# Performance work log

Measured on AMD Instinct MI355X. Metric: run time of the kernel, lower is better.

The kernel has to match this reference:

```python
import jax, jax.numpy as jnp
import numpy as np

N_GRAPHS = 8192
NODES_PER_GRAPH = 62
IN_CH = 4
HID = 64
NUM_CLASSES = 3
DEG = 8
N = N_GRAPHS * NODES_PER_GRAPH        # 507904 total nodes
E = N * DEG                            # 4063232 edges
BN_EPS = 1e-5


def setup_inputs() -> dict:
    key = jax.random.key(0)
    ks = jax.random.split(key, 24)

    def lin_w(k, i, o):
        return (jax.random.normal(k, (i, o), jnp.float32) / np.float32(np.sqrt(i)))

    inp = {
        "x": jax.random.normal(ks[0], (N, IN_CH), jnp.float32),
        "edge_src": jax.random.randint(ks[1], (E,), 0, N, dtype=jnp.int32),
        "edge_dst": jax.random.randint(ks[2], (E,), 0, N, dtype=jnp.int32),
        "num_graphs": N_GRAPHS,
        # conv1 MLP: Linear(4,64) -> ReLU -> Linear(64,64)
        "W1a": lin_w(ks[3], IN_CH, HID), "b1a": jnp.zeros((HID,), jnp.float32),
        "W1b": lin_w(ks[4], HID, HID),   "b1b": jnp.zeros((HID,), jnp.float32),
        "g1": jnp.ones((HID,), jnp.float32), "be1": jnp.zeros((HID,), jnp.float32),
        # conv2 MLP
        "W2a": lin_w(ks[5], HID, HID), "b2a": jnp.zeros((HID,), jnp.float32),
        "W2b": lin_w(ks[6], HID, HID), "b2b": jnp.zeros((HID,), jnp.float32),
        "g2": jnp.ones((HID,), jnp.float32), "be2": jnp.zeros((HID,), jnp.float32),
        # conv3 MLP
        "W3a": lin_w(ks[7], HID, HID), "b3a": jnp.zeros((HID,), jnp.float32),
        "W3b": lin_w(ks[8], HID, HID), "b3b": jnp.zeros((HID,), jnp.float32),
        "g3": jnp.ones((HID,), jnp.float32), "be3": jnp.zeros((HID,), jnp.float32),
        # final classifier fc2 (fc1 is unused in the original forward)
        "Wfc": lin_w(ks[9], HID, NUM_CLASSES), "bfc": jnp.zeros((NUM_CLASSES,), jnp.float32),
    }
    return inp


def _gin_conv(x, src, dst, Wa, ba, Wb, bb):
    # GINConv with eps=0: mlp(x_i + sum_{j->i} x_j)
    agg = jax.ops.segment_sum(x[src], dst, num_segments=N)
    h = x + agg
    return jnp.maximum(h @ Wa + ba, 0.0) @ Wb + bb


def _bn(h, g, b):
    # BatchNorm1d with batch statistics (training-mode math)
    m = h.mean(axis=0)
    v = h.var(axis=0)
    return (h - m) * jax.lax.rsqrt(v + BN_EPS) * g + b


def reference(x, edge_src, edge_dst, num_graphs,
              W1a, b1a, W1b, b1b, g1, be1,
              W2a, b2a, W2b, b2b, g2, be2,
              W3a, b3a, W3b, b3b, g3, be3,
              Wfc, bfc):
    h = _bn(jnp.maximum(_gin_conv(x, edge_src, edge_dst, W1a, b1a, W1b, b1b), 0.0), g1, be1)
    h = _bn(jnp.maximum(_gin_conv(h, edge_src, edge_dst, W2a, b2a, W2b, b2b), 0.0), g2, be2)
    h = _bn(jnp.maximum(_gin_conv(h, edge_src, edge_dst, W3a, b3a, W3b, b3b), 0.0), g3, be3)
    h = h.reshape(num_graphs, -1, HID).sum(axis=1)   # sum-pool nodes per graph
    # dropout is identity in eval mode
    return h @ Wfc + bfc
```

## Files before the change

### kernel.cpp

```cpp
#include <hip/hip_runtime.h>
#include <hip/hip_bf16.h>

#define NN   507904
#define NE   4063232
#define NG   8192
#define NPG  62
#define NPBLK 1984

#define NB    248
#define BRNG  2048
#define BCAP  17152
#define PBCAP 31744
#define P3BLK 992
#define CSRSZ (NB * PBCAP)

#define OFF_R     0
#define OFF_GSUM  (OFF_R + NN * 32 + 64)
#define OFF_PART  (OFF_GSUM + NG * 64)
#define OFF_AGGBF (OFF_R + NN * 64)
#define OFF_CSR   (OFF_AGGBF + NN * 32 + 32)
#define OFF_OC    (OFF_CSR + CSRSZ)
#define OFF_BCUR  (OFF_OC + 2 * NN)
#define OFF_WTB   (OFF_BCUR + 256)
#define OFF_SS    (OFF_WTB + 11264)

#define WB_W1B 0
#define WB_W2A 4096
#define WB_W2B 8192
#define WB_W3A 12288
#define WB_W3B 16384
#define WB_W1A 20480

typedef __attribute__((ext_vector_type(8))) short short8;
typedef __attribute__((ext_vector_type(4))) float f32x4;
typedef unsigned short ushort_t;

__device__ __forceinline__ ushort_t f2bf_bits(float f) {
  union { float f; unsigned u; } x; x.f = f;
  unsigned r = x.u + 0x7FFF + ((x.u >> 16) & 1);
  return (ushort_t)(r >> 16);
}
__device__ __forceinline__ float bfu(ushort_t u) {
  union { unsigned i; float f; } x; x.i = ((unsigned)u) << 16; return x.f;
}

__global__ __launch_bounds__(256) void prep_weights(
    const float* __restrict__ w1a, const float* __restrict__ w1b,
    const float* __restrict__ w2a, const float* __restrict__ w2b,
    const float* __restrict__ w3a, const float* __restrict__ w3b,
    ushort_t* __restrict__ wtb, int* __restrict__ bcur,
    unsigned* __restrict__ sent1, unsigned* __restrict__ sent2,
    float* __restrict__ gsum) {
  int b = blockIdx.x, tid = threadIdx.x;
  if (b == 0) {
    ushort_t* d = wtb + WB_W1A;
    for (int i = tid; i < 2048; i += 256) {
      int n = i >> 5, k = i & 31;
      d[i] = (k < 4) ? f2bf_bits(w1a[k * 64 + n]) : (ushort_t)0;
    }
  } else if (b == 6) {
    bcur[tid] = 0;
    if (tid < 32) { sent1[tid] = 0; sent2[tid] = 0; }
  } else if (b >= 7) {
    float* g = gsum + (size_t)(b - 7) * 1024;
#pragma unroll
    for (int k = 0; k < 4; ++k) g[k * 256 + tid] = 0.0f;
  } else {
    const float* s; ushort_t* d;
    switch (b) {
      case 1: s = w1b; d = wtb + WB_W1B; break;
      case 2: s = w2a; d = wtb + WB_W2A; break;
      case 3: s = w2b; d = wtb + WB_W2B; break;
      case 4: s = w3a; d = wtb + WB_W3A; break;
      default: s = w3b; d = wtb + WB_W3B; break;
    }
    for (int i = tid; i < 4096; i += 256) {
      int k = i >> 6, n = i & 63;
      d[n * 64 + k] = f2bf_bits(s[i]);
    }
  }
}

__global__ __launch_bounds__(256) void p3_bin(
    const int* __restrict__ src, const int* __restrict__ dst,
    int* __restrict__ bcur, uint2* __restrict__ recs) {
  __shared__ int histo[256];
  __shared__ int scan_s[256];
  __shared__ int base_s[256];
  __shared__ int cur_s[256];
  __shared__ uint2 buf[4096];
  const int tid = threadIdx.x;
  const int e0 = blockIdx.x * 4096;

  histo[tid] = 0;
  __syncthreads();

  int d_[16], s_[16];
#pragma unroll
  for (int k = 0; k < 16; ++k) {
    int e = e0 + k * 256 + tid;
    d_[k] = dst[e]; s_[k] = src[e];
    atomicAdd(&histo[d_[k] >> 11], 1);
  }
  __syncthreads();

  int v = histo[tid];
  scan_s[tid] = v; __syncthreads();
  for (int s = 1; s < 256; s <<= 1) {
    int add = (tid >= s) ? scan_s[tid - s] : 0;
    __syncthreads();
    scan_s[tid] += add;
    __syncthreads();
  }
  int excl = scan_s[tid] - v;
  if (tid < NB) base_s[tid] = atomicAdd(&bcur[tid], v);
  cur_s[tid] = excl;
  histo[tid] = excl;
  __syncthreads();

#pragma unroll
  for (int k = 0; k < 16; ++k) {
    int b = d_[k] >> 11;
    int p = atomicAdd(&cur_s[b], 1);
    uint2 r; r.x = (unsigned)d_[k]; r.y = (unsigned)s_[k];
    buf[p] = r;
  }
  __syncthreads();

  for (int i = tid; i < 4096; i += 256) {
    uint2 r = buf[i];
    int b = (int)(r.x >> 11);
    int g = base_s[b] + (i - histo[b]);
    if (g < BCAP) recs[(size_t)b * BCAP + g] = r;
  }
}

__global__ __launch_bounds__(1024) void p4_build(
    const uint2* __restrict__ recs, const int* __restrict__ bcur,
    int* __restrict__ csr, int2* __restrict__ oc) {
  __shared__ int lcnt[2048];
  __shared__ int pscan[1024];
  __shared__ int sstart[2048];
  __shared__ int scur[2048];
  const int b = blockIdx.x, tid = threadIdx.x;
  int m = bcur[b]; if (m > BCAP) m = BCAP;
  const int cbase = b * PBCAP;
  const int nbase = b << 11;
  const uint2* rp = recs + (size_t)b * BCAP;

  lcnt[tid] = 0; lcnt[1024 + tid] = 0;
  __syncthreads();
  for (int i = tid; i < m; i += 1024)
    atomicAdd(&lcnt[rp[i].x & (BRNG - 1)], 1);
  __syncthreads();

  int a0 = lcnt[2 * tid], a1 = lcnt[2 * tid + 1];
  int p0 = (a0 + 7) & ~7, p1 = (a1 + 7) & ~7;
  int ps = p0 + p1;
  pscan[tid] = ps; __syncthreads();
  for (int s = 1; s < 1024; s <<= 1) {
    int add = (tid >= s) ? pscan[tid - s] : 0;
    __syncthreads();
    pscan[tid] += add;
    __syncthreads();
  }
  int e0 = pscan[tid] - ps;
  sstart[2 * tid] = e0;          scur[2 * tid] = e0;
  sstart[2 * tid + 1] = e0 + p0; scur[2 * tid + 1] = e0 + p0;
  __syncthreads();

  {
    int2 r0; r0.x = cbase + sstart[tid];        r0.y = lcnt[tid];
    int2 r1; r1.x = cbase + sstart[1024 + tid]; r1.y = lcnt[1024 + tid];
    oc[nbase + tid] = r0;
    oc[nbase + 1024 + tid] = r1;
  }
  __syncthreads();

  for (int i = tid; i < m; i += 1024) {
    uint2 r = rp[i];
    int p = atomicAdd(&scur[r.x & (BRNG - 1)], 1);
    csr[cbase + p] = (int)r.y;
  }
  __syncthreads();

#pragma unroll
  for (int k = 0; k < 2; ++k) {
    int i = k * 1024 + tid;
    int st = sstart[i], d = lcnt[i], p = (d + 7) & ~7;
    for (int q = d; q < p; ++q) csr[cbase + st + q] = NN;
  }
}

__global__ __launch_bounds__(256) void gather1(
    const float4* __restrict__ x, const int* __restrict__ csr,
    const int2* __restrict__ oc, float4* __restrict__ tout) {
  int n = blockIdx.x * 256 + threadIdx.x;
  float4 a = x[n];
  int2 oc_ = oc[n];
  int off = oc_.x, deg = oc_.y;
  const int* cp = csr + off;
  int j = 0;
  for (; j + 4 <= deg; j += 4) {
    int s0 = cp[j], s1 = cp[j + 1], s2 = cp[j + 2], s3 = cp[j + 3];
    float4 v0 = x[s0], v1 = x[s1], v2 = x[s2], v3 = x[s3];
    a.x += v0.x + v1.x + v2.x + v3.x;
    a.y += v0.y + v1.y + v2.y + v3.y;
    a.z += v0.z + v1.z + v2.z + v3.z;
    a.w += v0.w + v1.w + v2.w + v3.w;
  }
  for (; j < deg; ++j) {
    float4 v = x[cp[j]];
    a.x += v.x; a.y += v.y; a.z += v.z; a.w += v.w;
  }
  tout[n] = a;
}

__global__ __launch_bounds__(256) void mlp_l1(
    const float4* __restrict__ tin,
    const ushort_t* __restrict__ WaTb,
    const float* __restrict__ ba,
    const ushort_t* __restrict__ WbTb,
    const float* __restrict__ bb,
    ushort_t* __restrict__ routb,
    float* __restrict__ part) {
  __shared__ __align__(16) ushort_t zt[4096];
  __shared__ float red[512];
  const int tid = threadIdx.x;
  const int wave = tid >> 6, lane = tid & 63;
  const int col = lane & 15, quad = lane >> 4;

  short8 bWa1[4], bWb[2][4];
#pragma unroll
  for (int nt = 0; nt < 4; ++nt) {
    bWa1[nt] = *(const short8*)(WaTb + (nt * 16 + col) * 32 + quad * 8);
#pragma unroll
    for (int k0 = 0; k0 < 2; ++k0)
      bWb[k0][nt] = *(const short8*)(WbTb + (nt * 16 + col) * 64 + k0 * 32 + quad * 8);
  }
  float ba_n[4], bb_n[4];
#pragma unroll
  for (int nt = 0; nt < 4; ++nt) {
    ba_n[nt] = ba[nt * 16 + col];
    bb_n[nt] = bb[nt * 16 + col];
  }

  const int wbase = wave * 1024;
  float scol[4] = {0, 0, 0, 0}, qcol[4] = {0, 0, 0, 0};

  for (int it = 0; it < 4; ++it) {
    const int tile = blockIdx.x * 256 + it * 64 + wave * 16;

    f32x4 acc1[4];
#pragma unroll
    for (int nt = 0; nt < 4; ++nt) acc1[nt] = (f32x4){0.f, 0.f, 0.f, 0.f};

    float4 t4 = tin[tile + col];
    short8 az = {0, 0, 0, 0, 0, 0, 0, 0};
    if (quad == 0) {
      az[0] = (short)f2bf_bits(t4.x);
      az[1] = (short)f2bf_bits(t4.y);
      az[2] = (short)f2bf_bits(t4.z);
      az[3] = (short)f2bf_bits(t4.w);
    }
#pragma unroll
    for (int nt = 0; nt < 4; ++nt)
      acc1[nt] = __builtin_amdgcn_mfma_f32_16x16x32_bf16(az, bWa1[nt], acc1[nt], 0, 0, 0);

#pragma unroll
    for (int nt = 0; nt < 4; ++nt) {
      int oblk = nt * 2 + (col >> 3);
#pragma unroll
      for (int r = 0; r < 4; ++r) {
        int row = quad * 4 + r;
        float z = fmaxf(acc1[nt][r] + ba_n[nt], 0.0f);
        zt[wbase + row * 64 + (((oblk ^ (row & 7)) << 3) | (col & 7))] = f2bf_bits(z);
      }
    }
    short8 az0 = *(const short8*)&zt[wbase + col * 64 + ((quad ^ (col & 7)) << 3)];
    short8 az1 = *(const short8*)&zt[wbase + col * 64 + (((4 + quad) ^ (col & 7)) << 3)];

    f32x4 acc2[4];
#pragma unroll
    for (int nt = 0; nt < 4; ++nt) acc2[nt] = (f32x4){0.f, 0.f, 0.f, 0.f};
#pragma unroll
    for (int nt = 0; nt < 4; ++nt) {
      acc2[nt] = __builtin_amdgcn_mfma_f32_16x16x32_bf16(az0, bWb[0][nt], acc2[nt], 0, 0, 0);
      acc2[nt] = __builtin_amdgcn_mfma_f32_16x16x32_bf16(az1, bWb[1][nt], acc2[nt], 0, 0, 0);
    }
#pragma unroll
    for (int nt = 0; nt < 4; ++nt) {
      int oblk = nt * 2 + (col >> 3);
#pragma unroll
      for (int r = 0; r < 4; ++r) {
        int rw = quad * 4 + r;
        float v = fmaxf(acc2[nt][r] + bb_n[nt], 0.0f);
        zt[wbase + rw * 64 + (((oblk ^ (rw & 7)) << 3) | (col & 7))] = f2bf_bits(v);
        scol[nt] += v; qcol[nt] += v * v;
      }
    }
    {
      const int R = lane >> 2, sp = lane & 3;
      short8 w0 = *(const short8*)&zt[wbase + R * 64 + (((sp * 2) ^ (R & 7)) << 3)];
      short8 w1 = *(const short8*)&zt[wbase + R * 64 + (((sp * 2 + 1) ^ (R & 7)) << 3)];
      ushort_t* dst = routb + (size_t)(tile + R) * 64 + sp * 16;
      *(short8*)dst = w0;
      *(short8*)(dst + 8) = w1;
    }
  }

#pragma unroll
  for (int nt = 0; nt < 4; ++nt) {
    float s = scol[nt], q = qcol[nt];
    s += __shfl_xor(s, 16); s += __shfl_xor(s, 32);
    q += __shfl_xor(q, 16); q += __shfl_xor(q, 32);
    if (quad == 0) {
      red[wave * 128 + nt * 16 + col] = s;
      red[wave * 128 + 64 + nt * 16 + col] = q;
    }
  }
  __syncthreads();
  if (tid < 128)
    part[blockIdx.x * 128 + tid] =
        red[tid] + red[128 + tid] + red[256 + tid] + red[384 + tid];
}

template <bool GS>
__global__ __launch_bounds__(256) void mlp_fused(
    const ushort_t* __restrict__ h,
    const int* __restrict__ csr, const int2* __restrict__ oc,
    const float* __restrict__ ss,
    const ushort_t* __restrict__ WaTb,
    const float* __restrict__ ba,
    const ushort_t* __restrict__ WbTb,
    const float* __restrict__ bb,
    ushort_t* __restrict__ routb, float* __restrict__ gsum_g,
    float* __restrict__ part) {
  __shared__ __align__(16) ushort_t zt[4096];
  __shared__ float red[512];
  __shared__ float ssl[128];
  __shared__ float gsum[GS ? 384 : 1];
  const int tid = threadIdx.x;
  const int wave = tid >> 6, lane = tid & 63;
  const int col = lane & 15, quad = lane >> 4;
  if (tid < 128) ssl[tid] = ss[tid];
  const int g0 = (blockIdx.x * 256) / 62;
  if (GS) {
    for (int i = tid; i < 384; i += 256) gsum[i] = 0.0f;
  }

  short8 bWa[2][4], bWb[2][4];
#pragma unroll
  for (int nt = 0; nt < 4; ++nt) {
#pragma unroll
    for (int k0 = 0; k0 < 2; ++k0) {
      bWa[k0][nt] = *(const short8*)(WaTb + (nt * 16 + col) * 64 + k0 * 32 + quad * 8);
      bWb[k0][nt] = *(const short8*)(WbTb + (nt * 16 + col) * 64 + k0 * 32 + quad * 8);
    }
  }
  float ba_n[4], bb_n[4];
#pragma unroll
  for (int nt = 0; nt < 4; ++nt) {
    ba_n[nt] = ba[nt * 16 + col];
    bb_n[nt] = bb[nt * 16 + col];
  }
  __syncthreads();

  const float* scA = ssl + quad * 8;
  const float* scB = ssl + 32 + quad * 8;
  const float* sfA = ssl + 64 + quad * 8;
  const float* sfB = ssl + 96 + quad * 8;

  const int wbase = wave * 1024;
  float scol[4] = {0, 0, 0, 0}, qcol[4] = {0, 0, 0, 0};

  for (int it = 0; it < 4; ++it) {
    const int tile = blockIdx.x * 256 + it * 64 + wave * 16;
    const int row = tile + col;
    const int2 o = oc[row];

    const ushort_t* hp = h + (size_t)(unsigned)row * 64u + quad * 8;
    short8 sl0 = *(const short8*)hp;
    short8 sl1 = *(const short8*)(hp + 32);
    float accA[8], accB[8];
#pragma unroll
    for (int e = 0; e < 8; ++e) {
      accA[e] = bfu((ushort_t)sl0[e]);
      accB[e] = bfu((ushort_t)sl1[e]);
    }

    const int chunks = (o.y + 7) >> 3;
    for (int c = 0; c < chunks; ++c) {
      const int* cp = csr + o.x + (c << 3);
      int4 i0 = *(const int4*)cp;
      int4 i1 = *(const int4*)(cp + 4);
      int idx[8] = {i0.x, i0.y, i0.z, i0.w, i1.x, i1.y, i1.z, i1.w};
#pragma unroll
      for (int j = 0; j < 8; ++j) {
        const ushort_t* p = h + (size_t)(unsigned)idx[j] * 64u + quad * 8;
        short8 l0 = *(const short8*)p;
        short8 l1 = *(const short8*)(p + 32);
#pragma unroll
        for (int e = 0; e < 8; ++e) {
          accA[e] += bfu((ushort_t)l0[e]);
          accB[e] += bfu((ushort_t)l1[e]);
        }
      }
    }

    const float m1 = (float)(o.y + 1);
    short8 a0, a1;
#pragma unroll
    for (int e = 0; e < 8; ++e) {
      a0[e] = (short)f2bf_bits(fmaf(scA[e], accA[e], m1 * sfA[e]));
      a1[e] = (short)f2bf_bits(fmaf(scB[e], accB[e], m1 * sfB[e]));
    }

    f32x4 acc1[4];
#pragma unroll
    for (int nt = 0; nt < 4; ++nt) acc1[nt] = (f32x4){0.f, 0.f, 0.f, 0.f};
#pragma unroll
    for (int nt = 0; nt < 4; ++nt) {
      acc1[nt] = __builtin_amdgcn_mfma_f32_16x16x32_bf16(a0, bWa[0][nt], acc1[nt], 0, 0, 0);
      acc1[nt] = __builtin_amdgcn_mfma_f32_16x16x32_bf16(a1, bWa[1][nt], acc1[nt], 0, 0, 0);
    }

#pragma unroll
    for (int nt = 0; nt < 4; ++nt) {
      int oblk = nt * 2 + (col >> 3);
#pragma unroll
      for (int r = 0; r < 4; ++r) {
        int rw = quad * 4 + r;
        float z = fmaxf(acc1[nt][r] + ba_n[nt], 0.0f);
        zt[wbase + rw * 64 + (((oblk ^ (rw & 7)) << 3) | (col & 7))] = f2bf_bits(z);
      }
    }
    short8 az0 = *(const short8*)&zt[wbase + col * 64 + ((quad ^ (col & 7)) << 3)];
    short8 az1 = *(const short8*)&zt[wbase + col * 64 + (((4 + quad) ^ (col & 7)) << 3)];

    f32x4 acc2[4];
#pragma unroll
    for (int nt = 0; nt < 4; ++nt) acc2[nt] = (f32x4){0.f, 0.f, 0.f, 0.f};
#pragma unroll
    for (int nt = 0; nt < 4; ++nt) {
      acc2[nt] = __builtin_amdgcn_mfma_f32_16x16x32_bf16(az0, bWb[0][nt], acc2[nt], 0, 0, 0);
      acc2[nt] = __builtin_amdgcn_mfma_f32_16x16x32_bf16(az1, bWb[1][nt], acc2[nt], 0, 0, 0);
    }

    if (GS) {
#pragma unroll
      for (int nt = 0; nt < 4; ++nt) {
#pragma unroll
        for (int r = 0; r < 4; ++r) {
          int rw = tile + quad * 4 + r;
          float v = fmaxf(acc2[nt][r] + bb_n[nt], 0.0f);
          scol[nt] += v; qcol[nt] += v * v;
          int gl = rw / 62 - g0;
          atomicAdd(&gsum[gl * 64 + nt * 16 + col], v);
        }
      }
    } else {
#pragma unroll
      for (int nt = 0; nt < 4; ++nt) {
        int oblk = nt * 2 + (col >> 3);
#pragma unroll
        for (int r = 0; r < 4; ++r) {
          int rw = quad * 4 + r;
          float v = fmaxf(acc2[nt][r] + bb_n[nt], 0.0f);
          zt[wbase + rw * 64 + (((oblk ^ (rw & 7)) << 3) | (col & 7))] = f2bf_bits(v);
          scol[nt] += v; qcol[nt] += v * v;
        }
      }
      const int R = lane >> 2, sp = lane & 3;
      short8 w0 = *(const short8*)&zt[wbase + R * 64 + (((sp * 2) ^ (R & 7)) << 3)];
      short8 w1 = *(const short8*)&zt[wbase + R * 64 + (((sp * 2 + 1) ^ (R & 7)) << 3)];
      ushort_t* dst = routb + (size_t)(tile + R) * 64 + sp * 16;
      *(short8*)dst = w0;
      *(short8*)(dst + 8) = w1;
    }
  }

#pragma unroll
  for (int nt = 0; nt < 4; ++nt) {
    float s = scol[nt], q = qcol[nt];
    s += __shfl_xor(s, 16); s += __shfl_xor(s, 32);
    q += __shfl_xor(q, 16); q += __shfl_xor(q, 32);
    if (quad == 0) {
      red[wave * 128 + nt * 16 + col] = s;
      red[wave * 128 + 64 + nt * 16 + col] = q;
    }
  }
  __syncthreads();
  if (tid < 128)
    part[blockIdx.x * 128 + tid] =
        red[tid] + red[128 + tid] + red[256 + tid] + red[384 + tid];

  if (GS) {
    for (int i = tid; i < 384; i += 256) {
      int g = g0 + (i >> 6);
      float v = gsum[i];
      if (g < NG && v != 0.0f) atomicAdd(&gsum_g[(size_t)g * 64 + (i & 63)], v);
    }
  }
}

__global__ __launch_bounds__(256) void reduce_finalize(
    const float* __restrict__ part, const float* __restrict__ gma,
    const float* __restrict__ bta, float* __restrict__ ss) {
  __shared__ double sh[512];
  const int c = blockIdx.x, tid = threadIdx.x;
  double a = 0.0, b = 0.0;
  for (int blk = tid; blk < NPBLK; blk += 256) {
    a += (double)part[blk * 128 + c];
    b += (double)part[blk * 128 + 64 + c];
  }
  sh[tid] = a; sh[256 + tid] = b;
  __syncthreads();
  for (int s = 128; s; s >>= 1) {
    if (tid < s) { sh[tid] += sh[tid + s]; sh[256 + tid] += sh[256 + tid + s]; }
    __syncthreads();
  }
  if (tid == 0) {
    double mean = sh[0] / (double)NN;
    double var = sh[256] / (double)NN - mean * mean;
    double sc = (double)gma[c] / sqrt(var + 1e-5);
    ss[c] = (float)sc;
    ss[64 + c] = (float)((double)bta[c] - mean * sc);
  }
}

__global__ __launch_bounds__(256) void fc_out(
    const float* __restrict__ gsum_g, const float* __restrict__ ss,
    const float* __restrict__ wfc, const float* __restrict__ bfc,
    float* __restrict__ out) {
  const int lane = threadIdx.x & 63;
  const int g = blockIdx.x * 4 + (threadIdx.x >> 6);
  const int c = lane;
  float s = gsum_g[(size_t)g * 64 + c];
  float pooled = fmaf(ss[c], s, (float)NPG * ss[64 + c]);
#pragma unroll
  for (int j = 0; j < 3; ++j) {
    float v = pooled * wfc[c * 3 + j];
    for (int m = 32; m; m >>= 1) v += __shfl_xor(v, m);
    if (c == 0) out[g * 3 + j] = v + bfc[j];
  }
}

extern "C" void kernel_launch(void* const* d_in, const int* in_sizes, int n_in,
                              void* d_out, int out_size, void* d_ws, size_t ws_size,
                              hipStream_t stream) {
  const float* x    = (const float*)d_in[0];
  const int*   srcE = (const int*)d_in[1];
  const int*   dstE = (const int*)d_in[2];
  const float* W1a = (const float*)d_in[4],  *b1a = (const float*)d_in[5];
  const float* W1b = (const float*)d_in[6],  *b1b = (const float*)d_in[7];
  const float* g1  = (const float*)d_in[8],  *be1 = (const float*)d_in[9];
  const float* W2a = (const float*)d_in[10], *b2a = (const float*)d_in[11];
  const float* W2b = (const float*)d_in[12], *b2b = (const float*)d_in[13];
  const float* g2  = (const float*)d_in[14], *be2 = (const float*)d_in[15];
  const float* W3a = (const float*)d_in[16], *b3a = (const float*)d_in[17];
  const float* W3b = (const float*)d_in[18], *b3b = (const float*)d_in[19];
  const float* g3  = (const float*)d_in[20], *be3 = (const float*)d_in[21];
  const float* Wfc = (const float*)d_in[22], *bfc = (const float*)d_in[23];

  float* ws = (float*)d_ws;
  ushort_t* Rb     = (ushort_t*)(ws + OFF_R);
  float*    GSUM   = ws + OFF_GSUM;
  float*    PART   = ws + OFF_PART;
  ushort_t* Ab     = (ushort_t*)(ws + OFF_AGGBF);
  void*     T1     = (void*)(ws + OFF_AGGBF);
  uint2*    RECS   = (uint2*)(ws + OFF_AGGBF);
  int*      CSR    = (int*)(ws + OFF_CSR);
  int2*     OC     = (int2*)(ws + OFF_OC);
  int*      BCUR   = (int*)(ws + OFF_BCUR);
  ushort_t* WTB    = (ushort_t*)(ws + OFF_WTB);
  float*    SS     = ws + OFF_SS;

  prep_weights<<<519, 256, 0, stream>>>(W1a, W1b, W2a, W2b, W3a, W3b, WTB, BCUR,
                                        (unsigned*)(Rb + (size_t)NN * 64),
                                        (unsigned*)(Ab + (size_t)NN * 64),
                                        GSUM);

  p3_bin<<<P3BLK, 256, 0, stream>>>(srcE, dstE, BCUR, RECS);
  p4_build<<<NB, 1024, 0, stream>>>(RECS, BCUR, CSR, OC);

  gather1<<<NN / 256, 256, 0, stream>>>((const float4*)x, CSR, OC, (float4*)T1);
  mlp_l1<<<NPBLK, 256, 0, stream>>>((const float4*)T1, WTB + WB_W1A, b1a,
                                    WTB + WB_W1B, b1b, Rb, PART);
  reduce_finalize<<<64, 256, 0, stream>>>(PART, g1, be1, SS + 0);

  mlp_fused<false><<<NPBLK, 256, 0, stream>>>(Rb, CSR, OC, SS + 0,
                                              WTB + WB_W2A, b2a,
                                              WTB + WB_W2B, b2b,
                                              Ab, nullptr, PART);
  reduce_finalize<<<64, 256, 0, stream>>>(PART, g2, be2, SS + 128);

  mlp_fused<true><<<NPBLK, 256, 0, stream>>>(Ab, CSR, OC, SS + 128,
                                             WTB + WB_W3A, b3a,
                                             WTB + WB_W3B, b3b,
                                             nullptr, GSUM, PART);
  reduce_finalize<<<64, 256, 0, stream>>>(PART, g3, be3, SS + 256);

  fc_out<<<NG / 4, 256, 0, stream>>>(GSUM, SS + 256, Wfc, bfc, (float*)d_out);
}
```

Measured before the change: 646.5 us.

## Stage MLP weights in LDS and reduce graph-pool atomics via shuffles

Moves the two 64x64 bf16 weight matrices from per-thread registers into padded shared memory (stride 72) and reads them per tile, with a launch bound requesting 5 blocks per SM, to lower VGPR pressure and raise occupancy. In the GS path, per-row LDS atomics into graph sums are replaced by splitting each 16-row tile into at most two graphs, reducing across quads with shuffles, and issuing one atomic per column per graph. This adds LDS traffic for weight reads each iteration and about 18KB more shared memory per block, which could itself limit occupancy.

Result: no change. 644.4 us (-0.3%).

```diff
diff --git a/kernel.cpp b/kernel.cpp
--- a/kernel.cpp
+++ b/kernel.cpp
@@ -326,7 +326,7 @@
 }
 
 template <bool GS>
-__global__ __launch_bounds__(256) void mlp_fused(
+__global__ __launch_bounds__(256, 5) void mlp_fused(
     const ushort_t* __restrict__ h,
     const int* __restrict__ csr, const int2* __restrict__ oc,
     const float* __restrict__ ss,
@@ -337,6 +337,8 @@
     ushort_t* __restrict__ routb, float* __restrict__ gsum_g,
     float* __restrict__ part) {
   __shared__ __align__(16) ushort_t zt[4096];
+  __shared__ __align__(16) ushort_t wa_l[4608];
+  __shared__ __align__(16) ushort_t wb_l[4608];
   __shared__ float red[512];
   __shared__ float ssl[128];
   __shared__ float gsum[GS ? 384 : 1];
@@ -348,16 +350,12 @@
   if (GS) {
     for (int i = tid; i < 384; i += 256) gsum[i] = 0.0f;
   }
-
-  short8 bWa[2][4], bWb[2][4];
-#pragma unroll
-  for (int nt = 0; nt < 4; ++nt) {
-#pragma unroll
-    for (int k0 = 0; k0 < 2; ++k0) {
-      bWa[k0][nt] = *(const short8*)(WaTb + (nt * 16 + col) * 64 + k0 * 32 + quad * 8);
-      bWb[k0][nt] = *(const short8*)(WbTb + (nt * 16 + col) * 64 + k0 * 32 + quad * 8);
-    }
-  }
+  for (int i = tid; i < 4096; i += 256) {
+    int n = i >> 6, k = i & 63;
+    wa_l[n * 72 + k] = WaTb[i];
+    wb_l[n * 72 + k] = WbTb[i];
+  }
+
   float ba_n[4], bb_n[4];
 #pragma unroll
   for (int nt = 0; nt < 4; ++nt) {
@@ -416,13 +414,20 @@
       a1[e] = (short)f2bf_bits(fmaf(scB[e], accB[e], m1 * sfB[e]));
     }
 
+    int wofs = 0;
+    asm volatile("" : "+v"(wofs));
+    const ushort_t* wap = wa_l + wofs;
+    const ushort_t* wbp = wb_l + wofs;
+
     f32x4 acc1[4];
 #pragma unroll
     for (int nt = 0; nt < 4; ++nt) acc1[nt] = (f32x4){0.f, 0.f, 0.f, 0.f};
 #pragma unroll
     for (int nt = 0; nt < 4; ++nt) {
-      acc1[nt] = __builtin_amdgcn_mfma_f32_16x16x32_bf16(a0, bWa[0][nt], acc1[nt], 0, 0, 0);
-      acc1[nt] = __builtin_amdgcn_mfma_f32_16x16x32_bf16(a1, bWa[1][nt], acc1[nt], 0, 0, 0);
+      short8 w0 = *(const short8*)(wap + (nt * 16 + col) * 72 + quad * 8);
+      short8 w1 = *(const short8*)(wap + (nt * 16 + col) * 72 + 32 + quad * 8);
+      acc1[nt] = __builtin_amdgcn_mfma_f32_16x16x32_bf16(a0, w0, acc1[nt], 0, 0, 0);
+      acc1[nt] = __builtin_amdgcn_mfma_f32_16x16x32_bf16(a1, w1, acc1[nt], 0, 0, 0);
     }
 
 #pragma unroll
@@ -443,11 +448,18 @@
     for (int nt = 0; nt < 4; ++nt) acc2[nt] = (f32x4){0.f, 0.f, 0.f, 0.f};
 #pragma unroll
     for (int nt = 0; nt < 4; ++nt) {
-      acc2[nt] = __builtin_amdgcn_mfma_f32_16x16x32_bf16(az0, bWb[0][nt], acc2[nt], 0, 0, 0);
-      acc2[nt] = __builtin_amdgcn_mfma_f32_16x16x32_bf16(az1, bWb[1][nt], acc2[nt], 0, 0, 0);
+      short8 w0 = *(const short8*)(wbp + (nt * 16 + col) * 72 + quad * 8);
+      short8 w1 = *(const short8*)(wbp + (nt * 16 + col) * 72 + 32 + quad * 8);
+      acc2[nt] = __builtin_amdgcn_mfma_f32_16x16x32_bf16(az0, w0, acc2[nt], 0, 0, 0);
+      acc2[nt] = __builtin_amdgcn_mfma_f32_16x16x32_bf16(az1, w1, acc2[nt], 0, 0, 0);
     }
 
     if (GS) {
+      const int gLo = tile / 62;
+      const int rEnd = (gLo + 1) * 62;
+      float vLo[4], vHi[4];
+#pragma unroll
+      for (int nt = 0; nt < 4; ++nt) { vLo[nt] = 0.f; vHi[nt] = 0.f; }
 #pragma unroll
       for (int nt = 0; nt < 4; ++nt) {
 #pragma unroll
@@ -455,8 +467,20 @@
           int rw = tile + quad * 4 + r;
           float v = fmaxf(acc2[nt][r] + bb_n[nt], 0.0f);
           scol[nt] += v; qcol[nt] += v * v;
-          int gl = rw / 62 - g0;
-          atomicAdd(&gsum[gl * 64 + nt * 16 + col], v);
+          if (rw < rEnd) vLo[nt] += v; else vHi[nt] += v;
+        }
+      }
+#pragma unroll
+      for (int nt = 0; nt < 4; ++nt) {
+        vLo[nt] += __shfl_xor(vLo[nt], 16); vLo[nt] += __shfl_xor(vLo[nt], 32);
+        vHi[nt] += __shfl_xor(vHi[nt], 16); vHi[nt] += __shfl_xor(vHi[nt], 32);
+      }
+      if (quad == 0) {
+        const int gl = gLo - g0;
+#pragma unroll
+        for (int nt = 0; nt < 4; ++nt) {
+          atomicAdd(&gsum[gl * 64 + nt * 16 + col], vLo[nt]);
+          atomicAdd(&gsum[(gl + 1) * 64 + nt * 16 + col], vHi[nt]);
         }
       }
     } else {
```
